# Optimization experiments

Hardware: AMD Instinct MI355X
Metric: run time of the kernel (lower is better)

Reference implementation:

```python
import jax, jax.numpy as jnp
import numpy as np

B, T = 48, 88200          # batch of 2 s clips at internal_sr=44100
N_EXC, N_LOOP = 6, 2      # exc_order+1, loop_order+1


def invert_lpc(y, A):
    """x[t] = y[t] + sum_{k=1..N} A[:, t, k-1] * y[t-k]  (zi = 0).
    y: (B,T), A: (B,T,N) -> (B,T). Vectorized time-varying FIR."""
    Bs, Ts = y.shape
    N = A.shape[2]
    yp = jnp.pad(y, ((0, 0), (N, 0)))  # N leading zeros = zero initial state
    # shifts[:, t, k-1] = y[t-k]
    shifts = jnp.stack([yp[:, N - k:N - k + Ts] for k in range(1, N + 1)], axis=2)
    return y + jnp.sum(A * shifts, axis=2)


def sample_wise_lpc(x, A):
    """Time-varying all-pole IIR: y[t] = x[t] - sum_{k=1..N} A[:, t, k-1]*y[t-k].
    Sequential recurrence over T via lax.scan. x: (B,T), A: (B,T,N)."""
    Bs, Ts = x.shape
    N = A.shape[2]

    def step(carry, inp):
        # carry: (B,N) = [y[t-1], ..., y[t-N]]
        xt, at = inp  # (B,), (B,N)
        yt = xt - jnp.sum(at * carry, axis=1)
        new_carry = jnp.concatenate([yt[:, None], carry[:, :-1]], axis=1)
        return new_carry, yt

    carry0 = jnp.zeros((Bs, N), x.dtype)
    _, ys = jax.lax.scan(step, carry0, (x.T, jnp.swapaxes(A, 0, 1)))
    return ys.T  # (B,T)


def setup_inputs() -> dict:
    key = jax.random.key(0)
    k1, k2, k3 = jax.random.split(key, 3)
    y = jax.random.normal(k1, (B, T), dtype=jnp.float32)
    # excitation (FIR-inverse) coefficients: mild, zero-centered
    A_exc = (jax.random.uniform(k2, (B, T, N_EXC), dtype=jnp.float32) - 0.5) * 0.2
    # loop (all-pole) coefficients kept small so the IIR recurrence is stable
    A_loop = (jax.random.uniform(k3, (B, T, N_LOOP), dtype=jnp.float32) - 0.5) * 0.5
    return {"y": y, "A_exc": A_exc, "A_loop": A_loop}


def reference(y, A_exc, A_loop):
    # Core DiffKS pipeline kernel: inverse LPC (feed-forward comb/loop inversion)
    # followed by the sample-wise recursive LPC resynthesis (Karplus-Strong loop).
    x = invert_lpc(y, A_exc)
    return sample_wise_lpc(x, A_loop)
```

## Files before the change

### kernel.cpp

```cpp
#include <hip/hip_runtime.h>


#define T_LEN 88200
#define B_N   48
#define OUT_W 480
#define WUP   32
#define NCH   184
#define WPB   4

__device__ __forceinline__ float4 zero4() { return make_float4(0.f, 0.f, 0.f, 0.f); }

__device__ __forceinline__ float4 ld_g(const float* __restrict__ p, int t) {
    if (t >= 0 && t + 3 < T_LEN) return *(const float4*)(p + t);
    return zero4();
}

__global__ __launch_bounds__(256, 4) void diffks_kernel(
    const float* __restrict__ y, const float* __restrict__ A_exc,
    const float* __restrict__ A_loop, float* __restrict__ out) {
    const int tid  = threadIdx.x;
    const int widx = tid >> 6;
    const int lane = tid & 63;
    const int w = blockIdx.x * WPB + widx;
    const int b = w / NCH;
    const int c = w - b * NCH;
    const int s  = c * OUT_W;
    const int t0 = s - WUP + 8 * lane;

    const float* yb  = y      + (size_t)b * T_LEN;
    const float* aeb = A_exc  + (size_t)b * T_LEN * 6;
    const float* alb = A_loop + (size_t)b * T_LEN * 2;
    float*       ob  = out    + (size_t)b * T_LEN;

    const bool full = (t0 >= 0) && (t0 < T_LEN);
    float4 ya, yc, ae[12], al[4];
    if (full) {
        const float4* py = (const float4*)(yb + t0);
        ya = py[0]; yc = py[1];
        const float4* pa = (const float4*)(aeb + (size_t)t0 * 6);
#pragma unroll
        for (int i = 0; i < 12; ++i) ae[i] = pa[i];
        const float4* pl = (const float4*)(alb + (size_t)t0 * 2);
#pragma unroll
        for (int i = 0; i < 4; ++i) al[i] = pl[i];
    } else {
        ya = yc = zero4();
#pragma unroll
        for (int i = 0; i < 12; ++i) ae[i] = zero4();
#pragma unroll
        for (int i = 0; i < 4; ++i) al[i] = zero4();
    }
    const float4 hm2 = ld_g(yb, t0 - 8);
    const float4 hm1 = ld_g(yb, t0 - 4);

    float yw[16] = { hm2.x, hm2.y, hm2.z, hm2.w, hm1.x, hm1.y, hm1.z, hm1.w,
                     ya.x,  ya.y,  ya.z,  ya.w,  yc.x,  yc.y,  yc.z,  yc.w };
    const float* aef = (const float*)ae;
    const float* alf = (const float*)al;

    float xs[8], a1s[8], a2s[8];
    float p00 = 1.f, p01 = 0.f, p10 = 0.f, p11 = 1.f, c0 = 0.f, c1 = 0.f;
#pragma unroll
    for (int j = 0; j < 8; ++j) {
        float xv = yw[8 + j];
#pragma unroll
        for (int k = 1; k <= 6; ++k)
            xv = fmaf(aef[j * 6 + (k - 1)], yw[8 + j - k], xv);
        xs[j] = xv;
        const float a1 = alf[2 * j], a2 = alf[2 * j + 1];
        a1s[j] = a1; a2s[j] = a2;
        const float n00 = fmaf(-a1, p00, -a2 * p10);
        const float n01 = fmaf(-a1, p01, -a2 * p11);
        p10 = p00; p11 = p01; p00 = n00; p01 = n01;
        const float nc0 = fmaf(-a1, c0, fmaf(-a2, c1, xv));
        c1 = c0; c0 = nc0;
    }

#pragma unroll
    for (int d = 1; d <= 2; d <<= 1) {
        const float q00 = __shfl_up(p00, d, 64), q01 = __shfl_up(p01, d, 64);
        const float q10 = __shfl_up(p10, d, 64), q11 = __shfl_up(p11, d, 64);
        const float qc0 = __shfl_up(c0, d, 64),  qc1 = __shfl_up(c1, d, 64);
        if (lane >= d) {
            const float m00 = fmaf(p00, q00, p01 * q10);
            const float m01 = fmaf(p00, q01, p01 * q11);
            const float m10 = fmaf(p10, q00, p11 * q10);
            const float m11 = fmaf(p10, q01, p11 * q11);
            const float nc0 = fmaf(p00, qc0, fmaf(p01, qc1, c0));
            const float nc1 = fmaf(p10, qc0, fmaf(p11, qc1, c1));
            p00 = m00; p01 = m01; p10 = m10; p11 = m11; c0 = nc0; c1 = nc1;
        }
    }
    {
        const float qc0 = __shfl_up(c0, 4, 64), qc1 = __shfl_up(c1, 4, 64);
        if (lane >= 4) {
            const float nc0 = fmaf(p00, qc0, fmaf(p01, qc1, c0));
            const float nc1 = fmaf(p10, qc0, fmaf(p11, qc1, c1));
            c0 = nc0; c1 = nc1;
        }
    }

    float y1 = __shfl_up(c0, 1, 64);
    float y2 = __shfl_up(c1, 1, 64);
    if (lane == 0) { y1 = 0.f; y2 = 0.f; }
    float ov[8];
#pragma unroll
    for (int j = 0; j < 8; ++j) {
        const float yt = fmaf(-a1s[j], y1, fmaf(-a2s[j], y2, xs[j]));
        y2 = y1; y1 = yt;
        ov[j] = yt;
    }

    if (lane >= WUP / 8 && t0 < T_LEN) {
        *(float4*)(ob + t0)     = make_float4(ov[0], ov[1], ov[2], ov[3]);
        *(float4*)(ob + t0 + 4) = make_float4(ov[4], ov[5], ov[6], ov[7]);
    }
}

extern "C" void kernel_launch(void* const* d_in, const int* in_sizes, int n_in,
                              void* d_out, int out_size, void* d_ws, size_t ws_size,
                              hipStream_t stream) {
    const float* y      = (const float*)d_in[0];
    const float* A_exc  = (const float*)d_in[1];
    const float* A_loop = (const float*)d_in[2];
    float* out = (float*)d_out;

    const int waves = B_N * NCH;
    const int grid  = waves / WPB;
    diffks_kernel<<<grid, 256, 0, stream>>>(y, A_exc, A_loop, out);
}
```

Measured before the change: 194.5 us.

## Process multiple sequential steps per wave with carried state and prefetch

Each wavefront now walks four consecutive 256-sample steps instead of one 512-sample chunk. It carries the IIR boundary state between steps via a lane-63 broadcast and composes it with the per-lane scan transforms. This shrinks the redundant warm-up overlap per output sample and prefetches the next step's inputs while computing the current one. In exchange, each wave runs more serial work, there are fewer waves overall, and holding the prefetched buffers raises register pressure.

```diff
diff --git a/kernel.cpp b/kernel.cpp
--- a/kernel.cpp
+++ b/kernel.cpp
@@ -3,16 +3,41 @@
 
 #define T_LEN 88200
 #define B_N   48
-#define OUT_W 480
 #define WUP   32
-#define NCH   184
+#define STEP  256
+#define NSTEP 4
+#define OUT_W 992
+#define NCHW  89
 #define WPB   4
+
+struct StepData { float4 yv, ae[6], al[2]; };
 
 __device__ __forceinline__ float4 zero4() { return make_float4(0.f, 0.f, 0.f, 0.f); }
 
 __device__ __forceinline__ float4 ld_g(const float* __restrict__ p, int t) {
     if (t >= 0 && t + 3 < T_LEN) return *(const float4*)(p + t);
     return zero4();
+}
+
+__device__ __forceinline__ StepData load_step(const float* __restrict__ yb,
+                                              const float* __restrict__ aeb,
+                                              const float* __restrict__ alb,
+                                              int t) {
+    StepData r;
+    if (t >= 0 && t + 3 < T_LEN) {
+        r.yv = *(const float4*)(yb + t);
+        const float4* pa = (const float4*)(aeb + (size_t)t * 6);
+#pragma unroll
+        for (int i = 0; i < 6; ++i) r.ae[i] = pa[i];
+        const float4* pl = (const float4*)(alb + (size_t)t * 2);
+        r.al[0] = pl[0]; r.al[1] = pl[1];
+    } else {
+        r.yv = zero4();
+#pragma unroll
+        for (int i = 0; i < 6; ++i) r.ae[i] = zero4();
+        r.al[0] = r.al[1] = zero4();
+    }
+    return r;
 }
 
 __global__ __launch_bounds__(256, 4) void diffks_kernel(
@@ -22,98 +47,98 @@
     const int widx = tid >> 6;
     const int lane = tid & 63;
     const int w = blockIdx.x * WPB + widx;
-    const int b = w / NCH;
-    const int c = w - b * NCH;
-    const int s  = c * OUT_W;
-    const int t0 = s - WUP + 8 * lane;
+    const int b = w / NCHW;
+    const int c = w - b * NCHW;
+    const int s = c * OUT_W;
 
     const float* yb  = y      + (size_t)b * T_LEN;
     const float* aeb = A_exc  + (size_t)b * T_LEN * 6;
     const float* alb = A_loop + (size_t)b * T_LEN * 2;
     float*       ob  = out    + (size_t)b * T_LEN;
 
-    const bool full = (t0 >= 0) && (t0 < T_LEN);
-    float4 ya, yc, ae[12], al[4];
-    if (full) {
-        const float4* py = (const float4*)(yb + t0);
-        ya = py[0]; yc = py[1];
-        const float4* pa = (const float4*)(aeb + (size_t)t0 * 6);
-#pragma unroll
-        for (int i = 0; i < 12; ++i) ae[i] = pa[i];
-        const float4* pl = (const float4*)(alb + (size_t)t0 * 2);
-#pragma unroll
-        for (int i = 0; i < 4; ++i) al[i] = pl[i];
-    } else {
-        ya = yc = zero4();
-#pragma unroll
-        for (int i = 0; i < 12; ++i) ae[i] = zero4();
-#pragma unroll
-        for (int i = 0; i < 4; ++i) al[i] = zero4();
-    }
-    const float4 hm2 = ld_g(yb, t0 - 8);
-    const float4 hm1 = ld_g(yb, t0 - 4);
-
-    float yw[16] = { hm2.x, hm2.y, hm2.z, hm2.w, hm1.x, hm1.y, hm1.z, hm1.w,
-                     ya.x,  ya.y,  ya.z,  ya.w,  yc.x,  yc.y,  yc.z,  yc.w };
-    const float* aef = (const float*)ae;
-    const float* alf = (const float*)al;
-
-    float xs[8], a1s[8], a2s[8];
-    float p00 = 1.f, p01 = 0.f, p10 = 0.f, p11 = 1.f, c0 = 0.f, c1 = 0.f;
-#pragma unroll
-    for (int j = 0; j < 8; ++j) {
-        float xv = yw[8 + j];
-#pragma unroll
-        for (int k = 1; k <= 6; ++k)
-            xv = fmaf(aef[j * 6 + (k - 1)], yw[8 + j - k], xv);
-        xs[j] = xv;
-        const float a1 = alf[2 * j], a2 = alf[2 * j + 1];
-        a1s[j] = a1; a2s[j] = a2;
-        const float n00 = fmaf(-a1, p00, -a2 * p10);
-        const float n01 = fmaf(-a1, p01, -a2 * p11);
-        p10 = p00; p11 = p01; p00 = n00; p01 = n01;
-        const float nc0 = fmaf(-a1, c0, fmaf(-a2, c1, xv));
-        c1 = c0; c0 = nc0;
-    }
+    int t = s - WUP + 4 * lane;
+    StepData cur = load_step(yb, aeb, alb, t);
+    float sc0 = 0.f, sc1 = 0.f;
 
 #pragma unroll
-    for (int d = 1; d <= 2; d <<= 1) {
-        const float q00 = __shfl_up(p00, d, 64), q01 = __shfl_up(p01, d, 64);
-        const float q10 = __shfl_up(p10, d, 64), q11 = __shfl_up(p11, d, 64);
-        const float qc0 = __shfl_up(c0, d, 64),  qc1 = __shfl_up(c1, d, 64);
-        if (lane >= d) {
-            const float m00 = fmaf(p00, q00, p01 * q10);
-            const float m01 = fmaf(p00, q01, p01 * q11);
-            const float m10 = fmaf(p10, q00, p11 * q10);
-            const float m11 = fmaf(p10, q01, p11 * q11);
-            const float nc0 = fmaf(p00, qc0, fmaf(p01, qc1, c0));
-            const float nc1 = fmaf(p10, qc0, fmaf(p11, qc1, c1));
-            p00 = m00; p01 = m01; p10 = m10; p11 = m11; c0 = nc0; c1 = nc1;
+    for (int k = 0; k < NSTEP; ++k) {
+        StepData nxt;
+        if (k < NSTEP - 1) nxt = load_step(yb, aeb, alb, t + STEP);
+
+        const float4 hm2 = ld_g(yb, t - 8);
+        const float4 hm1 = ld_g(yb, t - 4);
+        const float yw[12] = { hm2.x, hm2.y, hm2.z, hm2.w,
+                               hm1.x, hm1.y, hm1.z, hm1.w,
+                               cur.yv.x, cur.yv.y, cur.yv.z, cur.yv.w };
+        const float* aef = (const float*)cur.ae;
+        const float* alf = (const float*)cur.al;
+
+        float xs[4], a1s[4], a2s[4];
+        float p00 = 1.f, p01 = 0.f, p10 = 0.f, p11 = 1.f, c0 = 0.f, c1 = 0.f;
+#pragma unroll
+        for (int j = 0; j < 4; ++j) {
+            float xv = yw[8 + j];
+#pragma unroll
+            for (int kk = 1; kk <= 6; ++kk)
+                xv = fmaf(aef[j * 6 + (kk - 1)], yw[8 + j - kk], xv);
+            xs[j] = xv;
+            const float a1 = alf[2 * j], a2 = alf[2 * j + 1];
+            a1s[j] = a1; a2s[j] = a2;
+            const float n00 = fmaf(-a1, p00, -a2 * p10);
+            const float n01 = fmaf(-a1, p01, -a2 * p11);
+            p10 = p00; p11 = p01; p00 = n00; p01 = n01;
+            const float nc0 = fmaf(-a1, c0, fmaf(-a2, c1, xv));
+            c1 = c0; c0 = nc0;
         }
-    }
-    {
-        const float qc0 = __shfl_up(c0, 4, 64), qc1 = __shfl_up(c1, 4, 64);
-        if (lane >= 4) {
-            const float nc0 = fmaf(p00, qc0, fmaf(p01, qc1, c0));
-            const float nc1 = fmaf(p10, qc0, fmaf(p11, qc1, c1));
-            c0 = nc0; c1 = nc1;
+
+#pragma unroll
+        for (int d = 1; d <= 4; d <<= 1) {
+            const float q00 = __shfl_up(p00, d, 64), q01 = __shfl_up(p01, d, 64);
+            const float q10 = __shfl_up(p10, d, 64), q11 = __shfl_up(p11, d, 64);
+            const float qc0 = __shfl_up(c0, d, 64),  qc1 = __shfl_up(c1, d, 64);
+            if (lane >= d) {
+                const float m00 = fmaf(p00, q00, p01 * q10);
+                const float m01 = fmaf(p00, q01, p01 * q11);
+                const float m10 = fmaf(p10, q00, p11 * q10);
+                const float m11 = fmaf(p10, q01, p11 * q11);
+                const float nc0 = fmaf(p00, qc0, fmaf(p01, qc1, c0));
+                const float nc1 = fmaf(p10, qc0, fmaf(p11, qc1, c1));
+                p00 = m00; p01 = m01; p10 = m10; p11 = m11; c0 = nc0; c1 = nc1;
+            }
         }
-    }
+        {
+            const float qc0 = __shfl_up(c0, 8, 64), qc1 = __shfl_up(c1, 8, 64);
+            if (lane >= 8) {
+                const float nc0 = fmaf(p00, qc0, fmaf(p01, qc1, c0));
+                const float nc1 = fmaf(p10, qc0, fmaf(p11, qc1, c1));
+                c0 = nc0; c1 = nc1;
+            }
+        }
 
-    float y1 = __shfl_up(c0, 1, 64);
-    float y2 = __shfl_up(c1, 1, 64);
-    if (lane == 0) { y1 = 0.f; y2 = 0.f; }
-    float ov[8];
+        float e00 = __shfl_up(p00, 1, 64), e01 = __shfl_up(p01, 1, 64);
+        float e10 = __shfl_up(p10, 1, 64), e11 = __shfl_up(p11, 1, 64);
+        float ec0 = __shfl_up(c0, 1, 64),  ec1 = __shfl_up(c1, 1, 64);
+        if (lane == 0) { e00 = 1.f; e01 = 0.f; e10 = 0.f; e11 = 1.f;
+                         ec0 = 0.f; ec1 = 0.f; }
+        float y1 = fmaf(e00, sc0, fmaf(e01, sc1, ec0));
+        float y2 = fmaf(e10, sc0, fmaf(e11, sc1, ec1));
+
+        float ov[4];
 #pragma unroll
-    for (int j = 0; j < 8; ++j) {
-        const float yt = fmaf(-a1s[j], y1, fmaf(-a2s[j], y2, xs[j]));
-        y2 = y1; y1 = yt;
-        ov[j] = yt;
-    }
+        for (int j = 0; j < 4; ++j) {
+            const float yt = fmaf(-a1s[j], y1, fmaf(-a2s[j], y2, xs[j]));
+            y2 = y1; y1 = yt;
+            ov[j] = yt;
+        }
 
-    if (lane >= WUP / 8 && t0 < T_LEN) {
-        *(float4*)(ob + t0)     = make_float4(ov[0], ov[1], ov[2], ov[3]);
-        *(float4*)(ob + t0 + 4) = make_float4(ov[4], ov[5], ov[6], ov[7]);
+        sc0 = __shfl(y1, 63, 64);
+        sc1 = __shfl(y2, 63, 64);
+
+        if ((k > 0 || lane >= WUP / 4) && t < T_LEN)
+            *(float4*)(ob + t) = make_float4(ov[0], ov[1], ov[2], ov[3]);
+
+        t += STEP;
+        cur = nxt;
     }
 }
 
@@ -125,7 +150,7 @@
     const float* A_loop = (const float*)d_in[2];
     float* out = (float*)d_out;
 
-    const int waves = B_N * NCH;
+    const int waves = B_N * NCHW;
     const int grid  = waves / WPB;
     diffks_kernel<<<grid, 256, 0, stream>>>(y, A_exc, A_loop, out);
 }
```

Result: slower. 200.0 us (+2.8%).
